# Performance work log

Measured on AMD Instinct MI355X. Metric: run time of the kernel, lower is better.

The kernel has to match this reference:

```python
import jax, jax.numpy as jnp
import numpy as np

N = 50000          # nodes
E = 800000         # edges
F_IN, H, OUT = 512, 256, 2
BN_EPS = 1e-5


def setup_inputs() -> dict:
    key = jax.random.key(0)
    ks = jax.random.split(key, 10)
    x = jax.random.normal(ks[0], (N, F_IN), jnp.float32)
    edge_index = jax.random.randint(ks[1], (2, E), 0, N, dtype=jnp.int64)
    edge_weight = jax.random.uniform(ks[2], (E,), jnp.float32)

    def lin(k, fan_in, fan_out):
        return jax.random.normal(k, (fan_in, fan_out), jnp.float32) / np.sqrt(fan_in).astype(np.float32)

    W1, b1 = lin(ks[3], F_IN, H), jnp.zeros((H,), jnp.float32)
    W2, b2 = lin(ks[4], H, H), jnp.zeros((H,), jnp.float32)
    W3, b3 = lin(ks[5], H, OUT), jnp.zeros((OUT,), jnp.float32)
    # BatchNorm1d affine params + running stats (eval mode)
    g1, be1 = jnp.ones((H,), jnp.float32), jnp.zeros((H,), jnp.float32)
    m1 = 0.1 * jax.random.normal(ks[6], (H,), jnp.float32)
    v1 = jax.random.uniform(ks[7], (H,), jnp.float32, 0.5, 1.5)
    g2, be2 = jnp.ones((H,), jnp.float32), jnp.zeros((H,), jnp.float32)
    m2 = 0.1 * jax.random.normal(ks[8], (H,), jnp.float32)
    v2 = jax.random.uniform(ks[9], (H,), jnp.float32, 0.5, 1.5)
    return {"x": x, "edge_index": edge_index, "edge_weight": edge_weight,
            "W1": W1, "b1": b1, "g1": g1, "be1": be1, "m1": m1, "v1": v1,
            "W2": W2, "b2": b2, "g2": g2, "be2": be2, "m2": m2, "v2": v2,
            "W3": W3, "b3": b3}


def gcn_conv(x, row, col, w, W, b):
    # PyG GCNConv (eval): h = x @ W; out[col] += norm * h[row]; + b
    # row/col/w already include self-loops with weight 1.
    n = x.shape[0]
    h = x @ W                                      # [N, out]
    deg = jax.ops.segment_sum(w, col, num_segments=n)
    dinv = jnp.where(deg > 0, jax.lax.rsqrt(deg), 0.0)
    norm = dinv[row] * w * dinv[col]               # [E+N]
    out = jax.ops.segment_sum(h[row] * norm[:, None], col, num_segments=n)
    return out + b


def batchnorm_eval(x, g, be, m, v):
    return (x - m) * jax.lax.rsqrt(v + BN_EPS) * g + be


def reference(x, edge_index, edge_weight, W1, b1, g1, be1, m1, v1,
              W2, b2, g2, be2, m2, v2, W3, b3):
    n = x.shape[0]
    loops = jnp.arange(n, dtype=edge_index.dtype)
    row = jnp.concatenate([edge_index[0], loops])
    col = jnp.concatenate([edge_index[1], loops])
    w = jnp.concatenate([edge_weight, jnp.ones((n,), x.dtype)])

    h = jax.nn.relu(batchnorm_eval(gcn_conv(x, row, col, w, W1, b1), g1, be1, m1, v1))
    h = jax.nn.relu(batchnorm_eval(gcn_conv(h, row, col, w, W2, b2), g2, be2, m2, v2))
    return gcn_conv(h, row, col, w, W3, b3)
```

## Files before the change

kernel.cpp:

```cpp
#include <hip/hip_runtime.h>
#include <stdint.h>

#define F_IN 512
#define HF 256
#define OUT_F 2
#define BN_EPS 1e-5f
#define SCAN_B 256

typedef __attribute__((ext_vector_type(8))) short bf16x8;
typedef __attribute__((ext_vector_type(4))) float f32x4;

__device__ inline float bf2f(unsigned short u) {
    union { float f; uint32_t i; } v; v.i = ((uint32_t)u) << 16; return v.f;
}
__device__ inline unsigned short f2bf(float f) {
    union { float f; uint32_t i; } v; v.f = f;
    uint32_t r = v.i + 0x7FFFu + ((v.i >> 16) & 1u);
    return (unsigned short)(r >> 16);
}

__global__ void prep_kernel(unsigned long long* __restrict__ packed,
                            const float* __restrict__ W1, unsigned short* __restrict__ W1t,
                            const float* __restrict__ W2, unsigned short* __restrict__ W2t,
                            unsigned short* __restrict__ pad, int n, int padcount) {
    int idx = blockIdx.x * blockDim.x + threadIdx.x;
    if (idx < n) { packed[idx] = 1ULL << 20; return; }
    int j = idx - n;
    if (j < F_IN * HF) {
        int nn = j >> 9, k = j & (F_IN - 1);
        W1t[j] = f2bf(W1[(size_t)k * HF + nn]);
        return;
    }
    j -= F_IN * HF;
    if (j < HF * HF) {
        int nn = j >> 8, k = j & (HF - 1);
        W2t[j] = f2bf(W2[(size_t)k * HF + nn]);
        return;
    }
    j -= HF * HF;
    if (j < padcount) pad[j] = 0;
}

__global__ void count_pack_kernel(const int* __restrict__ col,
                                  const float* __restrict__ w,
                                  unsigned long long* __restrict__ packed, int e) {
    int i = blockIdx.x * blockDim.x + threadIdx.x;
    if (i < e) {
        unsigned long long add = (1ULL << 40)
            | (unsigned long long)__float2uint_rn(w[i] * 1048576.0f);
        atomicAdd(&packed[col[i]], add);
    }
}

__global__ void scan1_kernel(const unsigned long long* __restrict__ packed,
                             int* __restrict__ local, int* __restrict__ blocksum, int n) {
    __shared__ int tmp[SCAN_B];
    int i = blockIdx.x * SCAN_B + threadIdx.x;
    int v = (i < n) ? (int)(packed[i] >> 40) : 0;
    tmp[threadIdx.x] = v;
    __syncthreads();
    for (int off = 1; off < SCAN_B; off <<= 1) {
        int t = 0;
        if ((int)threadIdx.x >= off) t = tmp[threadIdx.x - off];
        __syncthreads();
        if ((int)threadIdx.x >= off) tmp[threadIdx.x] += t;
        __syncthreads();
    }
    if (i < n) local[i] = tmp[threadIdx.x] - v;
    if (threadIdx.x == SCAN_B - 1) blocksum[blockIdx.x] = tmp[SCAN_B - 1];
}

__global__ void scan3_dinv_kernel(int* __restrict__ csr_ptr, int* __restrict__ cursor,
                                  const int* __restrict__ blocksum,
                                  const unsigned long long* __restrict__ packed,
                                  float* __restrict__ dinv, int n, int e, int nb) {
    __shared__ int red[SCAN_B];
    int t = threadIdx.x;
    red[t] = (t < nb && t < (int)blockIdx.x) ? blocksum[t] : 0;
    __syncthreads();
    for (int off = SCAN_B / 2; off > 0; off >>= 1) {
        if (t < off) red[t] += red[t + off];
        __syncthreads();
    }
    int prefix = red[0];
    int i = blockIdx.x * SCAN_B + t;
    if (i < n) {
        int val = csr_ptr[i] + prefix;
        csr_ptr[i] = val;
        cursor[i] = val;
        unsigned long long pk = packed[i];
        float deg = (float)(pk & 0xFFFFFFFFFFULL) * (1.0f / 1048576.0f);
        dinv[i] = rsqrtf(deg);
    }
    if (i == 0) csr_ptr[n] = e;
}

__global__ void fill_kernel(const int* __restrict__ row, const int* __restrict__ col,
                            const float* __restrict__ w, const float* __restrict__ dinv,
                            int* __restrict__ cursor, int2* __restrict__ csr_edge, int e) {
    int i = blockIdx.x * blockDim.x + threadIdx.x;
    if (i < e) {
        int r = row[i], c = col[i];
        int pos = atomicAdd(&cursor[c], 1);
        float nrm = dinv[r] * w[i] * dinv[c];
        csr_edge[pos] = make_int2(r, __float_as_int(nrm));
    }
}

template<int A_IS_F32>
__global__ __launch_bounds__(256)
void gemm_bf16_kernel(const void* __restrict__ Araw,
                      const unsigned short* __restrict__ Bt,
                      unsigned short* __restrict__ C,
                      int Mvalid, int K, int Ntot) {
    __shared__ unsigned short As[128 * 40];
    __shared__ unsigned short Bs[64 * 40];
    const int tid  = threadIdx.x;
    const int lane = tid & 63;
    const int wv   = tid >> 6;
    const int m0 = blockIdx.x * 128;
    const int n0 = blockIdx.y * 64;

    const int sr = tid >> 2;
    const int sc = (tid & 3) * 8;

    f32x4 zero4 = {0.0f, 0.0f, 0.0f, 0.0f};
    f32x4 acc[2][4];
    #pragma unroll
    for (int i = 0; i < 2; ++i)
        #pragma unroll
        for (int j = 0; j < 4; ++j) acc[i][j] = zero4;

    const int q8 = (lane >> 4) * 8;
    const int ml = lane & 15;

    for (int k0 = 0; k0 < K; k0 += 32) {
        if (A_IS_F32) {
            const float* A = (const float*)Araw;
            #pragma unroll
            for (int h = 0; h < 2; ++h) {
                int rr = sr + h * 64;
                int gm = m0 + rr;
                float4 f0 = {0.f, 0.f, 0.f, 0.f}, f1 = {0.f, 0.f, 0.f, 0.f};
                if (gm < Mvalid) {
                    f0 = *(const float4*)(A + (size_t)gm * K + k0 + sc);
                    f1 = *(const float4*)(A + (size_t)gm * K + k0 + sc + 4);
                }
                bf16x8 v;
                v[0] = (short)f2bf(f0.x); v[1] = (short)f2bf(f0.y);
                v[2] = (short)f2bf(f0.z); v[3] = (short)f2bf(f0.w);
                v[4] = (short)f2bf(f1.x); v[5] = (short)f2bf(f1.y);
                v[6] = (short)f2bf(f1.z); v[7] = (short)f2bf(f1.w);
                *(bf16x8*)&As[rr * 40 + sc] = v;
            }
        } else {
            const unsigned short* A = (const unsigned short*)Araw;
            #pragma unroll
            for (int h = 0; h < 2; ++h) {
                int rr = sr + h * 64;
                int gm = m0 + rr;
                bf16x8 v = {0, 0, 0, 0, 0, 0, 0, 0};
                if (gm < Mvalid) v = *(const bf16x8*)(A + (size_t)gm * K + k0 + sc);
                *(bf16x8*)&As[rr * 40 + sc] = v;
            }
        }
        {
            bf16x8 v = *(const bf16x8*)(Bt + (size_t)(n0 + sr) * K + k0 + sc);
            *(bf16x8*)&Bs[sr * 40 + sc] = v;
        }
        __syncthreads();

        bf16x8 af[2], bfr[4];
        #pragma unroll
        for (int i = 0; i < 2; ++i)
            af[i] = *(const bf16x8*)&As[(wv * 32 + i * 16 + ml) * 40 + q8];
        #pragma unroll
        for (int j = 0; j < 4; ++j)
            bfr[j] = *(const bf16x8*)&Bs[(j * 16 + ml) * 40 + q8];
        #pragma unroll
        for (int i = 0; i < 2; ++i)
            #pragma unroll
            for (int j = 0; j < 4; ++j)
                acc[i][j] = __builtin_amdgcn_mfma_f32_16x16x32_bf16(af[i], bfr[j], acc[i][j], 0, 0, 0);
        __syncthreads();
    }

    const int q4 = (lane >> 4) * 4;
    #pragma unroll
    for (int i = 0; i < 2; ++i) {
        #pragma unroll
        for (int j = 0; j < 4; ++j) {
            #pragma unroll
            for (int rg = 0; rg < 4; ++rg) {
                int r = m0 + wv * 32 + i * 16 + q4 + rg;
                int c = n0 + j * 16 + ml;
                C[(size_t)r * Ntot + c] = f2bf(acc[i][j][rg]);
            }
        }
    }
}

__global__ void agg_bn_relu_kernel(const unsigned short* __restrict__ h,
                                   const int* __restrict__ ptr,
                                   const int2* __restrict__ edge,
                                   const float* __restrict__ dinv,
                                   const float* __restrict__ b, const float* __restrict__ g,
                                   const float* __restrict__ be, const float* __restrict__ m,
                                   const float* __restrict__ v,
                                   unsigned short* __restrict__ out, int n) {
    int wid  = (blockIdx.x * blockDim.x + threadIdx.x) >> 6;
    int lane = threadIdx.x & 63;
    if (wid >= n) return;
    int p0 = ptr[wid], p1 = ptr[wid + 1];
    const int fo = lane * 4;
    float a0 = 0.f, a1 = 0.f, a2 = 0.f, a3 = 0.f;

    for (int p = p0; p < p1; p += 8) {
        int   rr[8];
        float ww[8];
        #pragma unroll
        for (int k = 0; k < 8; ++k) {
            bool valid = (p + k) < p1;
            int2 e = edge[valid ? p + k : p0];
            rr[k] = e.x;
            ww[k] = valid ? __int_as_float(e.y) : 0.0f;
        }
        ushort4 hv[8];
        #pragma unroll
        for (int k = 0; k < 8; ++k)
            hv[k] = *(const ushort4*)(h + (size_t)rr[k] * HF + fo);
        #pragma unroll
        for (int k = 0; k < 8; ++k) {
            a0 += ww[k] * bf2f(hv[k].x);
            a1 += ww[k] * bf2f(hv[k].y);
            a2 += ww[k] * bf2f(hv[k].z);
            a3 += ww[k] * bf2f(hv[k].w);
        }
    }
    float s = dinv[wid];
    float sl = s * s;
    ushort4 hv = *(const ushort4*)(h + (size_t)wid * HF + fo);
    a0 += sl * bf2f(hv.x);
    a1 += sl * bf2f(hv.y);
    a2 += sl * bf2f(hv.z);
    a3 += sl * bf2f(hv.w);

    float4 bb  = *(const float4*)(b + fo);
    float4 gg  = *(const float4*)(g + fo);
    float4 bee = *(const float4*)(be + fo);
    float4 mm  = *(const float4*)(m + fo);
    float4 vv  = *(const float4*)(v + fo);
    ushort4 o;
    o.x = f2bf(fmaxf((a0 + bb.x - mm.x) * rsqrtf(vv.x + BN_EPS) * gg.x + bee.x, 0.f));
    o.y = f2bf(fmaxf((a1 + bb.y - mm.y) * rsqrtf(vv.y + BN_EPS) * gg.y + bee.y, 0.f));
    o.z = f2bf(fmaxf((a2 + bb.z - mm.z) * rsqrtf(vv.z + BN_EPS) * gg.z + bee.z, 0.f));
    o.w = f2bf(fmaxf((a3 + bb.w - mm.w) * rsqrtf(vv.w + BN_EPS) * gg.w + bee.w, 0.f));
    *(ushort4*)(out + (size_t)wid * HF + fo) = o;
}

__global__ void gemv_out_kernel(const unsigned short* __restrict__ a,
                                const float* __restrict__ W3,
                                float* __restrict__ h3, int n) {
    int gid = blockIdx.x * blockDim.x + threadIdx.x;
    int node = gid >> 6;
    int lane = gid & 63;
    if (node >= n) return;
    ushort4 av = *(const ushort4*)(a + (size_t)node * HF + lane * 4);
    float x0 = bf2f(av.x), x1 = bf2f(av.y), x2 = bf2f(av.z), x3 = bf2f(av.w);
    int k = lane * 4;
    float acc0 = x0 * W3[(k + 0) * 2 + 0] + x1 * W3[(k + 1) * 2 + 0]
               + x2 * W3[(k + 2) * 2 + 0] + x3 * W3[(k + 3) * 2 + 0];
    float acc1 = x0 * W3[(k + 0) * 2 + 1] + x1 * W3[(k + 1) * 2 + 1]
               + x2 * W3[(k + 2) * 2 + 1] + x3 * W3[(k + 3) * 2 + 1];
    #pragma unroll
    for (int o = 32; o > 0; o >>= 1) {
        acc0 += __shfl_down(acc0, o, 64);
        acc1 += __shfl_down(acc1, o, 64);
    }
    if (lane == 0) {
        h3[node * 2 + 0] = acc0;
        h3[node * 2 + 1] = acc1;
    }
}

__global__ void out_kernel(const float* __restrict__ h3,
                           const int* __restrict__ ptr, const int2* __restrict__ edge,
                           const float* __restrict__ dinv,
                           const float* __restrict__ b3, float* __restrict__ out, int n) {
    int i = blockIdx.x * blockDim.x + threadIdx.x;
    if (i >= n) return;
    int p0 = ptr[i], p1 = ptr[i + 1];
    float a0 = 0.f, a1 = 0.f;
    for (int p = p0; p < p1; p += 4) {
        #pragma unroll
        for (int k = 0; k < 4; ++k) {
            bool valid = (p + k) < p1;
            int2 e = edge[valid ? p + k : p0];
            float nw = valid ? __int_as_float(e.y) : 0.0f;
            float2 u = *(const float2*)(h3 + 2 * e.x);
            a0 += nw * u.x;
            a1 += nw * u.y;
        }
    }
    float s = dinv[i];
    float sl = s * s;
    out[2 * i + 0] = a0 + sl * h3[2 * i + 0] + b3[0];
    out[2 * i + 1] = a1 + sl * h3[2 * i + 1] + b3[1];
}

static inline char* align16(char* p) {
    return (char*)(((uintptr_t)p + 15) & ~(uintptr_t)15);
}

extern "C" void kernel_launch(void* const* d_in, const int* in_sizes, int n_in,
                              void* d_out, int out_size, void* d_ws, size_t ws_size,
                              hipStream_t stream) {
    const float* x   = (const float*)d_in[0];
    const int*   ei  = (const int*)d_in[1];
    const float* ew  = (const float*)d_in[2];
    const float* W1  = (const float*)d_in[3];
    const float* b1  = (const float*)d_in[4];
    const float* g1  = (const float*)d_in[5];
    const float* be1 = (const float*)d_in[6];
    const float* m1  = (const float*)d_in[7];
    const float* v1  = (const float*)d_in[8];
    const float* W2  = (const float*)d_in[9];
    const float* b2  = (const float*)d_in[10];
    const float* g2  = (const float*)d_in[11];
    const float* be2 = (const float*)d_in[12];
    const float* m2  = (const float*)d_in[13];
    const float* v2  = (const float*)d_in[14];
    const float* W3  = (const float*)d_in[15];
    const float* b3  = (const float*)d_in[16];

    const int N  = in_sizes[0] / F_IN;
    const int E  = in_sizes[2];
    const int MP = (N + 127) & ~127;
    const int* row = ei;
    const int* col = ei + E;

    char* wsb = (char*)d_ws;
    unsigned long long* packed = (unsigned long long*)wsb; wsb = align16(wsb + (size_t)N * 8);
    float* dinv     = (float*)wsb;          wsb = align16(wsb + (size_t)N * 4);
    int*   csr_ptr  = (int*)wsb;            wsb = align16(wsb + (size_t)(N + 1) * 4);
    int*   cursor   = (int*)wsb;            wsb = align16(wsb + (size_t)N * 4);
    int*   blocksum = (int*)wsb;            wsb = align16(wsb + (size_t)SCAN_B * 4);
    int2*  csr_edge = (int2*)wsb;           wsb = align16(wsb + (size_t)E * 8);
    unsigned short* W1t = (unsigned short*)wsb;  wsb = align16(wsb + (size_t)F_IN * HF * 2);
    unsigned short* W2t = (unsigned short*)wsb;  wsb = align16(wsb + (size_t)HF * HF * 2);
    unsigned short* bufh = (unsigned short*)wsb; wsb = align16(wsb + (size_t)MP * HF * 2);
    unsigned short* bufa = (unsigned short*)wsb; wsb = align16(wsb + (size_t)MP * HF * 2);
    float* h3 = (float*)wsb;                wsb = align16(wsb + (size_t)N * OUT_F * 4);
    float* outf = (float*)d_out;

    const int TB = 256;
    const int nscan = (N + SCAN_B - 1) / SCAN_B;
    const int padcount = (MP - N) * HF;
    const int preptot = N + F_IN * HF + HF * HF + padcount;

    prep_kernel<<<(preptot + TB - 1) / TB, TB, 0, stream>>>(
        packed, W1, W1t, W2, W2t, bufa + (size_t)N * HF, N, padcount);

    count_pack_kernel<<<(E + TB - 1) / TB, TB, 0, stream>>>(col, ew, packed, E);
    scan1_kernel<<<nscan, SCAN_B, 0, stream>>>(packed, csr_ptr, blocksum, N);
    scan3_dinv_kernel<<<nscan, SCAN_B, 0, stream>>>(csr_ptr, cursor, blocksum, packed, dinv, N, E, nscan);
    fill_kernel<<<(E + TB - 1) / TB, TB, 0, stream>>>(row, col, ew, dinv, cursor, csr_edge, E);

    dim3 ggrid(MP / 128, HF / 64);

    gemm_bf16_kernel<1><<<ggrid, TB, 0, stream>>>(x, W1t, bufh, N, F_IN, HF);
    agg_bn_relu_kernel<<<((size_t)N * 64 + TB - 1) / TB, TB, 0, stream>>>(
        bufh, csr_ptr, csr_edge, dinv, b1, g1, be1, m1, v1, bufa, N);

    gemm_bf16_kernel<0><<<ggrid, TB, 0, stream>>>(bufa, W2t, bufh, MP, HF, HF);
    agg_bn_relu_kernel<<<((size_t)N * 64 + TB - 1) / TB, TB, 0, stream>>>(
        bufh, csr_ptr, csr_edge, dinv, b2, g2, be2, m2, v2, bufa, N);

    gemv_out_kernel<<<((size_t)N * 64 + TB - 1) / TB, TB, 0, stream>>>(bufa, W3, h3, N);
    out_kernel<<<(N + TB - 1) / TB, TB, 0, stream>>>(h3, csr_ptr, csr_edge, dinv, b3, outf, N);
}
```

Measured before the change: 523.5 us.

## Fuse degree counting into GEMM1, fold output GEMV into second aggregation

Degree/weight counting atomics now run as extra blocks of the first GEMM launch, so the two overlap and one launch disappears. The final BN+ReLU aggregation computes the 2-wide W3 projection in-register with a wave reduction, removing the separate GEMV pass over the hidden activations. The LDS row stride is shortened from 40 to 36 elements, the aggregation loop gets a tail-free main body, and zeroing of the padding rows is dropped. Risks: the 36-element stride leaves 16-byte LDS vector accesses misaligned, and the padding rows of the second GEMM's input are left uninitialised; their outputs are never read.

```diff
diff --git a/kernel.cpp b/kernel.cpp
--- a/kernel.cpp
+++ b/kernel.cpp
@@ -6,6 +6,7 @@
 #define OUT_F 2
 #define BN_EPS 1e-5f
 #define SCAN_B 256
+#define LDSTR 36
 
 typedef __attribute__((ext_vector_type(8))) short bf16x8;
 typedef __attribute__((ext_vector_type(4))) float f32x4;
@@ -22,7 +23,7 @@
 __global__ void prep_kernel(unsigned long long* __restrict__ packed,
                             const float* __restrict__ W1, unsigned short* __restrict__ W1t,
                             const float* __restrict__ W2, unsigned short* __restrict__ W2t,
-                            unsigned short* __restrict__ pad, int n, int padcount) {
+                            int n) {
     int idx = blockIdx.x * blockDim.x + threadIdx.x;
     if (idx < n) { packed[idx] = 1ULL << 20; return; }
     int j = idx - n;
@@ -35,91 +36,19 @@
     if (j < HF * HF) {
         int nn = j >> 8, k = j & (HF - 1);
         W2t[j] = f2bf(W2[(size_t)k * HF + nn]);
-        return;
-    }
-    j -= HF * HF;
-    if (j < padcount) pad[j] = 0;
-}
-
-__global__ void count_pack_kernel(const int* __restrict__ col,
-                                  const float* __restrict__ w,
-                                  unsigned long long* __restrict__ packed, int e) {
-    int i = blockIdx.x * blockDim.x + threadIdx.x;
-    if (i < e) {
-        unsigned long long add = (1ULL << 40)
-            | (unsigned long long)__float2uint_rn(w[i] * 1048576.0f);
-        atomicAdd(&packed[col[i]], add);
-    }
-}
-
-__global__ void scan1_kernel(const unsigned long long* __restrict__ packed,
-                             int* __restrict__ local, int* __restrict__ blocksum, int n) {
-    __shared__ int tmp[SCAN_B];
-    int i = blockIdx.x * SCAN_B + threadIdx.x;
-    int v = (i < n) ? (int)(packed[i] >> 40) : 0;
-    tmp[threadIdx.x] = v;
-    __syncthreads();
-    for (int off = 1; off < SCAN_B; off <<= 1) {
-        int t = 0;
-        if ((int)threadIdx.x >= off) t = tmp[threadIdx.x - off];
-        __syncthreads();
-        if ((int)threadIdx.x >= off) tmp[threadIdx.x] += t;
-        __syncthreads();
-    }
-    if (i < n) local[i] = tmp[threadIdx.x] - v;
-    if (threadIdx.x == SCAN_B - 1) blocksum[blockIdx.x] = tmp[SCAN_B - 1];
-}
-
-__global__ void scan3_dinv_kernel(int* __restrict__ csr_ptr, int* __restrict__ cursor,
-                                  const int* __restrict__ blocksum,
-                                  const unsigned long long* __restrict__ packed,
-                                  float* __restrict__ dinv, int n, int e, int nb) {
-    __shared__ int red[SCAN_B];
-    int t = threadIdx.x;
-    red[t] = (t < nb && t < (int)blockIdx.x) ? blocksum[t] : 0;
-    __syncthreads();
-    for (int off = SCAN_B / 2; off > 0; off >>= 1) {
-        if (t < off) red[t] += red[t + off];
-        __syncthreads();
-    }
-    int prefix = red[0];
-    int i = blockIdx.x * SCAN_B + t;
-    if (i < n) {
-        int val = csr_ptr[i] + prefix;
-        csr_ptr[i] = val;
-        cursor[i] = val;
-        unsigned long long pk = packed[i];
-        float deg = (float)(pk & 0xFFFFFFFFFFULL) * (1.0f / 1048576.0f);
-        dinv[i] = rsqrtf(deg);
-    }
-    if (i == 0) csr_ptr[n] = e;
-}
-
-__global__ void fill_kernel(const int* __restrict__ row, const int* __restrict__ col,
-                            const float* __restrict__ w, const float* __restrict__ dinv,
-                            int* __restrict__ cursor, int2* __restrict__ csr_edge, int e) {
-    int i = blockIdx.x * blockDim.x + threadIdx.x;
-    if (i < e) {
-        int r = row[i], c = col[i];
-        int pos = atomicAdd(&cursor[c], 1);
-        float nrm = dinv[r] * w[i] * dinv[c];
-        csr_edge[pos] = make_int2(r, __float_as_int(nrm));
     }
 }
 
 template<int A_IS_F32>
-__global__ __launch_bounds__(256)
-void gemm_bf16_kernel(const void* __restrict__ Araw,
-                      const unsigned short* __restrict__ Bt,
-                      unsigned short* __restrict__ C,
-                      int Mvalid, int K, int Ntot) {
-    __shared__ unsigned short As[128 * 40];
-    __shared__ unsigned short Bs[64 * 40];
+__device__ __forceinline__
+void gemm_body(const void* __restrict__ Araw, const unsigned short* __restrict__ Bt,
+               unsigned short* __restrict__ C, int Mvalid, int K, int Ntot, int bid,
+               unsigned short* As, unsigned short* Bs) {
     const int tid  = threadIdx.x;
     const int lane = tid & 63;
     const int wv   = tid >> 6;
-    const int m0 = blockIdx.x * 128;
-    const int n0 = blockIdx.y * 64;
+    const int m0 = (bid >> 2) * 128;
+    const int n0 = (bid & 3) * 64;
 
     const int sr = tid >> 2;
     const int sc = (tid & 3) * 8;
@@ -151,7 +80,7 @@
                 v[2] = (short)f2bf(f0.z); v[3] = (short)f2bf(f0.w);
                 v[4] = (short)f2bf(f1.x); v[5] = (short)f2bf(f1.y);
                 v[6] = (short)f2bf(f1.z); v[7] = (short)f2bf(f1.w);
-                *(bf16x8*)&As[rr * 40 + sc] = v;
+                *(bf16x8*)&As[rr * LDSTR + sc] = v;
             }
         } else {
             const unsigned short* A = (const unsigned short*)Araw;
@@ -161,22 +90,22 @@
                 int gm = m0 + rr;
                 bf16x8 v = {0, 0, 0, 0, 0, 0, 0, 0};
                 if (gm < Mvalid) v = *(const bf16x8*)(A + (size_t)gm * K + k0 + sc);
-                *(bf16x8*)&As[rr * 40 + sc] = v;
+                *(bf16x8*)&As[rr * LDSTR + sc] = v;
             }
         }
         {
             bf16x8 v = *(const bf16x8*)(Bt + (size_t)(n0 + sr) * K + k0 + sc);
-            *(bf16x8*)&Bs[sr * 40 + sc] = v;
+            *(bf16x8*)&Bs[sr * LDSTR + sc] = v;
         }
         __syncthreads();
 
         bf16x8 af[2], bfr[4];
         #pragma unroll
         for (int i = 0; i < 2; ++i)
-            af[i] = *(const bf16x8*)&As[(wv * 32 + i * 16 + ml) * 40 + q8];
+            af[i] = *(const bf16x8*)&As[(wv * 32 + i * 16 + ml) * LDSTR + q8];
         #pragma unroll
         for (int j = 0; j < 4; ++j)
-            bfr[j] = *(const bf16x8*)&Bs[(j * 16 + ml) * 40 + q8];
+            bfr[j] = *(const bf16x8*)&Bs[(j * 16 + ml) * LDSTR + q8];
         #pragma unroll
         for (int i = 0; i < 2; ++i)
             #pragma unroll
@@ -200,14 +129,103 @@
     }
 }
 
-__global__ void agg_bn_relu_kernel(const unsigned short* __restrict__ h,
-                                   const int* __restrict__ ptr,
-                                   const int2* __restrict__ edge,
-                                   const float* __restrict__ dinv,
-                                   const float* __restrict__ b, const float* __restrict__ g,
-                                   const float* __restrict__ be, const float* __restrict__ m,
-                                   const float* __restrict__ v,
-                                   unsigned short* __restrict__ out, int n) {
+__global__ __launch_bounds__(256)
+void gemm1_count_kernel(const float* __restrict__ x, const unsigned short* __restrict__ W1t,
+                        unsigned short* __restrict__ C,
+                        const int* __restrict__ col, const float* __restrict__ w,
+                        unsigned long long* __restrict__ packed,
+                        int Mvalid, int e, int ngemm) {
+    __shared__ unsigned short As[128 * LDSTR];
+    __shared__ unsigned short Bs[64 * LDSTR];
+    int bid = blockIdx.x;
+    if (bid < ngemm) {
+        gemm_body<1>(x, W1t, C, Mvalid, F_IN, HF, bid, As, Bs);
+    } else {
+        int base = (bid - ngemm) * 1024 + (int)threadIdx.x;
+        #pragma unroll
+        for (int k = 0; k < 4; ++k) {
+            int i = base + k * 256;
+            if (i < e) {
+                unsigned long long add = (1ULL << 40)
+                    | (unsigned long long)__float2uint_rn(w[i] * 1048576.0f);
+                atomicAdd(&packed[col[i]], add);
+            }
+        }
+    }
+}
+
+__global__ __launch_bounds__(256)
+void gemm2_kernel(const unsigned short* __restrict__ A, const unsigned short* __restrict__ Bt,
+                  unsigned short* __restrict__ C, int Mvalid) {
+    __shared__ unsigned short As[128 * LDSTR];
+    __shared__ unsigned short Bs[64 * LDSTR];
+    gemm_body<0>(A, Bt, C, Mvalid, HF, HF, blockIdx.x, As, Bs);
+}
+
+__global__ void scan1_kernel(const unsigned long long* __restrict__ packed,
+                             int* __restrict__ local, int* __restrict__ blocksum, int n) {
+    __shared__ int tmp[SCAN_B];
+    int i = blockIdx.x * SCAN_B + threadIdx.x;
+    int v = (i < n) ? (int)(packed[i] >> 40) : 0;
+    tmp[threadIdx.x] = v;
+    __syncthreads();
+    for (int off = 1; off < SCAN_B; off <<= 1) {
+        int t = 0;
+        if ((int)threadIdx.x >= off) t = tmp[threadIdx.x - off];
+        __syncthreads();
+        if ((int)threadIdx.x >= off) tmp[threadIdx.x] += t;
+        __syncthreads();
+    }
+    if (i < n) local[i] = tmp[threadIdx.x] - v;
+    if (threadIdx.x == SCAN_B - 1) blocksum[blockIdx.x] = tmp[SCAN_B - 1];
+}
+
+__global__ void scan3_dinv_kernel(int* __restrict__ csr_ptr, int* __restrict__ cursor,
+                                  const int* __restrict__ blocksum,
+                                  const unsigned long long* __restrict__ packed,
+                                  float* __restrict__ dinv, int n, int e, int nb) {
+    __shared__ int red[SCAN_B];
+    int t = threadIdx.x;
+    red[t] = (t < nb && t < (int)blockIdx.x) ? blocksum[t] : 0;
+    __syncthreads();
+    for (int off = SCAN_B / 2; off > 0; off >>= 1) {
+        if (t < off) red[t] += red[t + off];
+        __syncthreads();
+    }
+    int prefix = red[0];
+    int i = blockIdx.x * SCAN_B + t;
+    if (i < n) {
+        int val = csr_ptr[i] + prefix;
+        csr_ptr[i] = val;
+        cursor[i] = val;
+        float deg = (float)(packed[i] & 0xFFFFFFFFFFULL) * (1.0f / 1048576.0f);
+        dinv[i] = rsqrtf(deg);
+    }
+    if (i == 0) csr_ptr[n] = e;
+}
+
+__global__ void fill_kernel(const int* __restrict__ row, const int* __restrict__ col,
+                            const float* __restrict__ w, const float* __restrict__ dinv,
+                            int* __restrict__ cursor, int2* __restrict__ csr_edge, int e) {
+    int i = blockIdx.x * blockDim.x + threadIdx.x;
+    if (i < e) {
+        int r = row[i], c = col[i];
+        int pos = atomicAdd(&cursor[c], 1);
+        float nrm = dinv[r] * w[i] * dinv[c];
+        csr_edge[pos] = make_int2(r, __float_as_int(nrm));
+    }
+}
+
+template<int FINAL>
+__global__ void agg_kernel(const unsigned short* __restrict__ h,
+                           const int* __restrict__ ptr,
+                           const int2* __restrict__ edge,
+                           const float* __restrict__ dinv,
+                           const float* __restrict__ b, const float* __restrict__ g,
+                           const float* __restrict__ be, const float* __restrict__ m,
+                           const float* __restrict__ v,
+                           unsigned short* __restrict__ out,
+                           const float* __restrict__ W3, float* __restrict__ h3, int n) {
     int wid  = (blockIdx.x * blockDim.x + threadIdx.x) >> 6;
     int lane = threadIdx.x & 63;
     if (wid >= n) return;
@@ -215,26 +233,43 @@
     const int fo = lane * 4;
     float a0 = 0.f, a1 = 0.f, a2 = 0.f, a3 = 0.f;
 
-    for (int p = p0; p < p1; p += 8) {
-        int   rr[8];
-        float ww[8];
+    const int pend = p0 + ((p1 - p0) & ~7);
+    for (int p = p0; p < pend; p += 8) {
+        int2 ed[8];
+        #pragma unroll
+        for (int k = 0; k < 8; ++k) ed[k] = edge[p + k];
+        ushort4 hv[8];
+        #pragma unroll
+        for (int k = 0; k < 8; ++k)
+            hv[k] = *(const ushort4*)(h + (size_t)ed[k].x * HF + fo);
         #pragma unroll
         for (int k = 0; k < 8; ++k) {
-            bool valid = (p + k) < p1;
-            int2 e = edge[valid ? p + k : p0];
-            rr[k] = e.x;
-            ww[k] = valid ? __int_as_float(e.y) : 0.0f;
+            float nw = __int_as_float(ed[k].y);
+            a0 += nw * bf2f(hv[k].x);
+            a1 += nw * bf2f(hv[k].y);
+            a2 += nw * bf2f(hv[k].z);
+            a3 += nw * bf2f(hv[k].w);
+        }
+    }
+    if (pend < p1) {
+        int2 ed[8];
+        float wv[8];
+        #pragma unroll
+        for (int k = 0; k < 8; ++k) {
+            int idx = pend + k < p1 ? pend + k : p1 - 1;
+            ed[k] = edge[idx];
+            wv[k] = (pend + k < p1) ? __int_as_float(ed[k].y) : 0.0f;
         }
         ushort4 hv[8];
         #pragma unroll
         for (int k = 0; k < 8; ++k)
-            hv[k] = *(const ushort4*)(h + (size_t)rr[k] * HF + fo);
+            hv[k] = *(const ushort4*)(h + (size_t)ed[k].x * HF + fo);
         #pragma unroll
         for (int k = 0; k < 8; ++k) {
-            a0 += ww[k] * bf2f(hv[k].x);
-            a1 += ww[k] * bf2f(hv[k].y);
-            a2 += ww[k] * bf2f(hv[k].z);
-            a3 += ww[k] * bf2f(hv[k].w);
+            a0 += wv[k] * bf2f(hv[k].x);
+            a1 += wv[k] * bf2f(hv[k].y);
+            a2 += wv[k] * bf2f(hv[k].z);
+            a3 += wv[k] * bf2f(hv[k].w);
         }
     }
     float s = dinv[wid];
@@ -250,36 +285,29 @@
     float4 bee = *(const float4*)(be + fo);
     float4 mm  = *(const float4*)(m + fo);
     float4 vv  = *(const float4*)(v + fo);
-    ushort4 o;
-    o.x = f2bf(fmaxf((a0 + bb.x - mm.x) * rsqrtf(vv.x + BN_EPS) * gg.x + bee.x, 0.f));
-    o.y = f2bf(fmaxf((a1 + bb.y - mm.y) * rsqrtf(vv.y + BN_EPS) * gg.y + bee.y, 0.f));
-    o.z = f2bf(fmaxf((a2 + bb.z - mm.z) * rsqrtf(vv.z + BN_EPS) * gg.z + bee.z, 0.f));
-    o.w = f2bf(fmaxf((a3 + bb.w - mm.w) * rsqrtf(vv.w + BN_EPS) * gg.w + bee.w, 0.f));
-    *(ushort4*)(out + (size_t)wid * HF + fo) = o;
-}
-
-__global__ void gemv_out_kernel(const unsigned short* __restrict__ a,
-                                const float* __restrict__ W3,
-                                float* __restrict__ h3, int n) {
-    int gid = blockIdx.x * blockDim.x + threadIdx.x;
-    int node = gid >> 6;
-    int lane = gid & 63;
-    if (node >= n) return;
-    ushort4 av = *(const ushort4*)(a + (size_t)node * HF + lane * 4);
-    float x0 = bf2f(av.x), x1 = bf2f(av.y), x2 = bf2f(av.z), x3 = bf2f(av.w);
-    int k = lane * 4;
-    float acc0 = x0 * W3[(k + 0) * 2 + 0] + x1 * W3[(k + 1) * 2 + 0]
-               + x2 * W3[(k + 2) * 2 + 0] + x3 * W3[(k + 3) * 2 + 0];
-    float acc1 = x0 * W3[(k + 0) * 2 + 1] + x1 * W3[(k + 1) * 2 + 1]
-               + x2 * W3[(k + 2) * 2 + 1] + x3 * W3[(k + 3) * 2 + 1];
-    #pragma unroll
-    for (int o = 32; o > 0; o >>= 1) {
-        acc0 += __shfl_down(acc0, o, 64);
-        acc1 += __shfl_down(acc1, o, 64);
-    }
-    if (lane == 0) {
-        h3[node * 2 + 0] = acc0;
-        h3[node * 2 + 1] = acc1;
+    float f0 = fmaxf((a0 + bb.x - mm.x) * rsqrtf(vv.x + BN_EPS) * gg.x + bee.x, 0.f);
+    float f1 = fmaxf((a1 + bb.y - mm.y) * rsqrtf(vv.y + BN_EPS) * gg.y + bee.y, 0.f);
+    float f2 = fmaxf((a2 + bb.z - mm.z) * rsqrtf(vv.z + BN_EPS) * gg.z + bee.z, 0.f);
+    float f3 = fmaxf((a3 + bb.w - mm.w) * rsqrtf(vv.w + BN_EPS) * gg.w + bee.w, 0.f);
+
+    if (!FINAL) {
+        ushort4 o;
+        o.x = f2bf(f0); o.y = f2bf(f1); o.z = f2bf(f2); o.w = f2bf(f3);
+        *(ushort4*)(out + (size_t)wid * HF + fo) = o;
+    } else {
+        float4 w0 = *(const float4*)(W3 + fo * 2);
+        float4 w1 = *(const float4*)(W3 + fo * 2 + 4);
+        float s0 = f0 * w0.x + f1 * w0.z + f2 * w1.x + f3 * w1.z;
+        float s1 = f0 * w0.y + f1 * w0.w + f2 * w1.y + f3 * w1.w;
+        #pragma unroll
+        for (int o = 32; o > 0; o >>= 1) {
+            s0 += __shfl_down(s0, o, 64);
+            s1 += __shfl_down(s1, o, 64);
+        }
+        if (lane == 0) {
+            h3[wid * 2 + 0] = s0;
+            h3[wid * 2 + 1] = s1;
+        }
     }
 }
 
@@ -294,9 +322,9 @@
     for (int p = p0; p < p1; p += 4) {
         #pragma unroll
         for (int k = 0; k < 4; ++k) {
-            bool valid = (p + k) < p1;
-            int2 e = edge[valid ? p + k : p0];
-            float nw = valid ? __int_as_float(e.y) : 0.0f;
+            int idx = p + k < p1 ? p + k : p1 - 1;
+            int2 e = edge[idx];
+            float nw = (p + k < p1) ? __int_as_float(e.y) : 0.0f;
             float2 u = *(const float2*)(h3 + 2 * e.x);
             a0 += nw * u.x;
             a1 += nw * u.y;
@@ -355,27 +383,26 @@
 
     const int TB = 256;
     const int nscan = (N + SCAN_B - 1) / SCAN_B;
-    const int padcount = (MP - N) * HF;
-    const int preptot = N + F_IN * HF + HF * HF + padcount;
-
-    prep_kernel<<<(preptot + TB - 1) / TB, TB, 0, stream>>>(
-        packed, W1, W1t, W2, W2t, bufa + (size_t)N * HF, N, padcount);
-
-    count_pack_kernel<<<(E + TB - 1) / TB, TB, 0, stream>>>(col, ew, packed, E);
+    const int preptot = N + F_IN * HF + HF * HF;
+    const int ngemm = (MP / 128) * 4;
+    const int ncount = (E + 1023) / 1024;
+
+    prep_kernel<<<(preptot + TB - 1) / TB, TB, 0, stream>>>(packed, W1, W1t, W2, W2t, N);
+
+    gemm1_count_kernel<<<ngemm + ncount, TB, 0, stream>>>(
+        x, W1t, bufh, col, ew, packed, N, E, ngemm);
+
     scan1_kernel<<<nscan, SCAN_B, 0, stream>>>(packed, csr_ptr, blocksum, N);
     scan3_dinv_kernel<<<nscan, SCAN_B, 0, stream>>>(csr_ptr, cursor, blocksum, packed, dinv, N, E, nscan);
     fill_kernel<<<(E + TB - 1) / TB, TB, 0, stream>>>(row, col, ew, dinv, cursor, csr_edge, E);
 
-    dim3 ggrid(MP / 128, HF / 64);
-
-    gemm_bf16_kernel<1><<<ggrid, TB, 0, stream>>>(x, W1t, bufh, N, F_IN, HF);
-    agg_bn_relu_kernel<<<((size_t)N * 64 + TB - 1) / TB, TB, 0, stream>>>(
-        bufh, csr_ptr, csr_edge, dinv, b1, g1, be1, m1, v1, bufa, N);
-
-    gemm_bf16_kernel<0><<<ggrid, TB, 0, stream>>>(bufa, W2t, bufh, MP, HF, HF);
-    agg_bn_relu_kernel<<<((size_t)N * 64 + TB - 1) / TB, TB, 0, stream>>>(
-        bufh, csr_ptr, csr_edge, dinv, b2, g2, be2, m2, v2, bufa, N);
-
-    gemv_out_kernel<<<((size_t)N * 64 + TB - 1) / TB, TB, 0, stream>>>(bufa, W3, h3, N);
+    agg_kernel<0><<<((size_t)N * 64 + TB - 1) / TB, TB, 0, stream>>>(
+        bufh, csr_ptr, csr_edge, dinv, b1, g1, be1, m1, v1, bufa, nullptr, nullptr, N);
+
+    gemm2_kernel<<<ngemm, TB, 0, stream>>>(bufa, W2t, bufh, MP);
+
+    agg_kernel<1><<<((size_t)N * 64 + TB - 1) / TB, TB, 0, stream>>>(
+        bufh, csr_ptr, csr_edge, dinv, b2, g2, be2, m2, v2, nullptr, W3, h3, N);
+
     out_kernel<<<(N + TB - 1) / TB, TB, 0, stream>>>(h3, csr_ptr, csr_edge, dinv, b3, outf, N);
 }
```

After: 528.7 us. No clear change (+1.0%).
